# Kernel tuning notes

Hardware: AMD Instinct MI355X
Metric: run time of the kernel (lower is better)

Reference implementation:

```python
import jax, jax.numpy as jnp
import numpy as np

B, N, F_NODE = 4, 50000, 64
E = 1600000
C, F_COL = 1000, 32
H = 16


def setup_inputs() -> dict:
    key = jax.random.key(0)
    ks = jax.random.split(key, 16)
    s = 0.1
    return {
        "node_features": jax.random.normal(ks[0], (B, N, F_NODE), jnp.float32),
        "col_features": jax.random.normal(ks[1], (B, C, F_COL), jnp.float32),
        "edge_index": jax.random.randint(ks[2], (2, E), 0, N, jnp.int32),
        "W1": jax.random.normal(ks[3], (F_NODE, H), jnp.float32) * s,
        "b1": jnp.zeros((H,), jnp.float32),
        "W2": jax.random.normal(ks[4], (H, H), jnp.float32) * s,
        "b2": jnp.zeros((H,), jnp.float32),
        "node_fc_W": jax.random.normal(ks[5], (H, 1), jnp.float32) * s,
        "node_fc_b": jnp.zeros((1,), jnp.float32),
        "col_W1": jax.random.normal(ks[6], (F_COL, H), jnp.float32) * s,
        "col_b1": jnp.zeros((H,), jnp.float32),
        "col_W2": jax.random.normal(ks[7], (H, 1), jnp.float32) * s,
        "col_b2": jnp.zeros((1,), jnp.float32),
        "fc_W": jax.random.normal(ks[8], (2, H), jnp.float32) * s,
        "fc_b": jnp.zeros((H,), jnp.float32),
        "out_W": jax.random.normal(ks[9], (H, 1), jnp.float32) * s,
        "out_b": jnp.zeros((1,), jnp.float32),
    }


def _gcn_conv(x, src, dst, W, b, num_nodes):
    # PyG GCNConv: x' = D^-1/2 (A+I) D^-1/2 (x W) + b
    x = x @ W
    loops = jnp.arange(num_nodes, dtype=src.dtype)
    s = jnp.concatenate([src, loops])
    d = jnp.concatenate([dst, loops])
    deg = jax.ops.segment_sum(jnp.ones_like(d, x.dtype), d, num_segments=num_nodes)
    dinv = jnp.where(deg > 0, jax.lax.rsqrt(deg), 0.0)
    norm = dinv[s] * dinv[d]                     # [E']
    msg = x[s] * norm[:, None]                   # gather + scale
    out = jax.ops.segment_sum(msg, d, num_segments=num_nodes)  # scatter-add
    return out + b


def reference(node_features, col_features, edge_index, W1, b1, W2, b2,
              node_fc_W, node_fc_b, col_W1, col_b1, col_W2, col_b2,
              fc_W, fc_b, out_W, out_b):
    Bs, Nn, Fn = node_features.shape
    num_nodes = Bs * Nn
    x = node_features.reshape(num_nodes, Fn)
    # faithful to torch: edge_index.expand(B,2,E).reshape(2,-1) (indices NOT offset per batch)
    Ee = edge_index.shape[1]
    ei = jnp.broadcast_to(edge_index, (Bs, 2, Ee)).reshape(2, Bs * Ee)
    src, dst = ei[0], ei[1]
    x = jax.nn.relu(_gcn_conv(x, src, dst, W1, b1, num_nodes))
    x = jax.nn.relu(_gcn_conv(x, src, dst, W2, b2, num_nodes))
    x = x.reshape(Bs, Nn, -1)
    node_out = (x @ node_fc_W + node_fc_b)[..., 0]          # [B, N]
    h = jax.nn.relu(col_features @ col_W1 + col_b1)
    col_out = (h @ col_W2 + col_b2)[..., 0]                 # [B, C]
    node_avg = node_out.mean(axis=1)[:, None]               # [B, 1]
    col_avg = col_out.mean(axis=1)[:, None]                 # [B, 1]
    combined = jnp.concatenate([node_avg, col_avg], axis=1)  # [B, 2]
    z = jax.nn.relu(combined @ fc_W + fc_b)
    return z @ out_W + out_b                                # [B, 1]
```

## Files before the change

kernel.cpp:

```cpp
#include <hip/hip_runtime.h>

static constexpr int NN   = 50000;
static constexpr int NBAT = 4;
static constexpr int NE   = 1600000;
static constexpr int NC   = 1000;
static constexpr int FN   = 64;
static constexpr int FCOL = 32;
static constexpr int HD   = 16;

static constexpr int NP     = 20;
static constexpr int PNODES = 2500;
static constexpr int PCAP   = 88000;
static constexpr int NSUB   = 1000;
static constexpr int SNODES = 50;
static constexpr int SCAP   = 2048;
static constexpr int SPP    = 50;
static constexpr int SLICES = 44;
static constexpr int CHUNK  = 4096;
static constexpr int CHUNK2 = 2048;

static constexpr int P1B  = (NE + CHUNK - 1) / CHUNK;
static constexpr int MLPB = (NN + 127) / 128;
static constexpr int COLB = 16;

__device__ inline float block_reduce_256(float v) {
    __shared__ float s[4];
    int lane = threadIdx.x & 63, wid = threadIdx.x >> 6;
    #pragma unroll
    for (int o = 32; o > 0; o >>= 1) v += __shfl_down(v, o);
    if (lane == 0) s[wid] = v;
    __syncthreads();
    if (threadIdx.x == 0) {
        float t = 0.f;
        #pragma unroll
        for (int i = 0; i < 4; i++) t += s[i];
        return t;
    }
    return 0.f;
}

__device__ inline float dot4(float4 a, float4 w) {
    return (a.x * w.x + a.y * w.y) + (a.z * w.z + a.w * w.w);
}

__device__ inline float4 quad_reduce_scatter(const float (&p)[16], int q) {
    constexpr int KA[8] = {0,1,2,3,8,9,10,11};
    constexpr int KB[8] = {4,5,6,7,12,13,14,15};
    bool hi1 = (q & 1);
    float m[8];
    #pragma unroll
    for (int i = 0; i < 8; i++) {
        float send = hi1 ? p[KA[i]] : p[KB[i]];
        float recv = __shfl_xor(send, 1);
        m[i] = (hi1 ? p[KB[i]] : p[KA[i]]) + recv;
    }
    bool hi2 = (q & 2);
    float r0, r1, r2, r3;
    {
        float s0 = hi2 ? m[0] : m[4];
        float s1 = hi2 ? m[1] : m[5];
        float s2 = hi2 ? m[2] : m[6];
        float s3 = hi2 ? m[3] : m[7];
        float v0 = __shfl_xor(s0, 2);
        float v1 = __shfl_xor(s1, 2);
        float v2 = __shfl_xor(s2, 2);
        float v3 = __shfl_xor(s3, 2);
        r0 = (hi2 ? m[4] : m[0]) + v0;
        r1 = (hi2 ? m[5] : m[1]) + v1;
        r2 = (hi2 ? m[6] : m[2]) + v2;
        r3 = (hi2 ? m[7] : m[3]) + v3;
    }
    return make_float4(r0, r1, r2, r3);
}

__device__ inline float mlp_tail(float4 t, int q, bool valid, const float* sw2,
                                 float4 bv, float4 b2v, float4 nfv) {
    float h0 = fmaxf(t.x + bv.x, 0.f);
    float h1 = fmaxf(t.y + bv.y, 0.f);
    float h2 = fmaxf(t.z + bv.z, 0.f);
    float h3 = fmaxf(t.w + bv.w, 0.f);
    float pk[16];
    const float* r0p = &sw2[(q * 4 + 0) * 20];
    const float* r1p = &sw2[(q * 4 + 1) * 20];
    const float* r2p = &sw2[(q * 4 + 2) * 20];
    const float* r3p = &sw2[(q * 4 + 3) * 20];
    #pragma unroll
    for (int k4 = 0; k4 < 4; k4++) {
        float4 w0 = *(const float4*)&r0p[k4 * 4];
        float4 w1 = *(const float4*)&r1p[k4 * 4];
        float4 w2 = *(const float4*)&r2p[k4 * 4];
        float4 w3 = *(const float4*)&r3p[k4 * 4];
        pk[k4*4+0] = h0 * w0.x + h1 * w1.x + h2 * w2.x + h3 * w3.x;
        pk[k4*4+1] = h0 * w0.y + h1 * w1.y + h2 * w2.y + h3 * w3.y;
        pk[k4*4+2] = h0 * w0.z + h1 * w1.z + h2 * w2.z + h3 * w3.z;
        pk[k4*4+3] = h0 * w0.w + h1 * w1.w + h2 * w2.w + h3 * w3.w;
    }
    float4 f = quad_reduce_scatter(pk, q);
    float sv = fmaxf(f.x + b2v.x, 0.f) * nfv.x
             + fmaxf(f.y + b2v.y, 0.f) * nfv.y
             + fmaxf(f.z + b2v.z, 0.f) * nfv.z
             + fmaxf(f.w + b2v.w, 0.f) * nfv.w;
    return valid ? sv : 0.f;
}

__global__ void __launch_bounds__(256) k_mega(
        const float* __restrict__ x, const int* __restrict__ src,
        const int* __restrict__ dst, const float* __restrict__ col,
        const float* __restrict__ W1, const float* __restrict__ b1,
        const float* __restrict__ W2, const float* __restrict__ b2,
        const float* __restrict__ nfcW,
        const float* __restrict__ cW1, const float* __restrict__ cb1,
        const float* __restrict__ cW2,
        int* __restrict__ gcur, unsigned* __restrict__ buf1,
        float* __restrict__ y1, double* __restrict__ sums) {
    __shared__ int ph[NP], pg[NP], pl[NP];
    __shared__ float swt[HD * FN];
    __shared__ float sw2[HD * 20];
    __shared__ float sb1[HD], sb2[HD], snf[HD];
    __shared__ float cw1s[FCOL * HD], csb1[HD], csw2[HD];

    int tid = threadIdx.x;
    int idx = blockIdx.x;

    if (idx < P1B) {
        if (tid < NP) ph[tid] = 0;
        __syncthreads();
        int e0 = idx * CHUNK;
        unsigned ent[16]; int bin[16];
        #pragma unroll
        for (int k = 0; k < 16; k++) {
            int e = e0 + k * 256 + tid;
            if (e < NE) {
                unsigned d = (unsigned)dst[e], s = (unsigned)src[e];
                ent[k] = (d << 16) | s;
                bin[k] = (int)(d / (unsigned)PNODES);
                atomicAdd(&ph[bin[k]], 1);
            } else bin[k] = -1;
        }
        __syncthreads();
        if (tid < NP) { pg[tid] = atomicAdd(&gcur[tid], ph[tid]); pl[tid] = 0; }
        __syncthreads();
        #pragma unroll
        for (int k = 0; k < 16; k++) {
            if (bin[k] >= 0) {
                int p = pg[bin[k]] + atomicAdd(&pl[bin[k]], 1);
                if (p < PCAP) buf1[(size_t)bin[k] * PCAP + p] = ent[k];
            }
        }
        return;
    }

    if (idx < P1B + NBAT * MLPB) {
        int t = idx - P1B;
        int b = t / MLPB, nb = t - b * MLPB;
        int q = tid & 3;
        int n0 = nb * 128 + (tid >> 2) * 2;
        bool v0 = (n0 < NN), v1 = (n0 + 1 < NN);
        const float* xb = x + (size_t)b * NN * FN;

        float4 a0, a1, a2, a3, c0, c1, c2, c3;
        a0 = a1 = a2 = a3 = c0 = c1 = c2 = c3 = make_float4(0.f, 0.f, 0.f, 0.f);
        if (v0) {
            const float4* p = (const float4*)(xb + (size_t)n0 * FN + q * 16);
            a0 = p[0]; a1 = p[1]; a2 = p[2]; a3 = p[3];
        }
        if (v1) {
            const float4* p = (const float4*)(xb + (size_t)(n0 + 1) * FN + q * 16);
            c0 = p[0]; c1 = p[1]; c2 = p[2]; c3 = p[3];
        }

        #pragma unroll
        for (int i = tid; i < HD * FN; i += 256) {
            int j = i >> 6, k = i & 63;
            swt[i] = W1[k * HD + j];
        }
        if (tid < HD * HD) sw2[(tid >> 4) * 20 + (tid & 15)] = W2[tid];
        if (tid < HD) { sb1[tid] = b1[tid]; sb2[tid] = b2[tid]; snf[tid] = nfcW[tid]; }
        __syncthreads();

        float p0[16], p1[16];
        #pragma unroll
        for (int j = 0; j < HD; j++) {
            const float4* w = (const float4*)&swt[j * FN + q * 16];
            float4 w0 = w[0], w1 = w[1], w2 = w[2], w3 = w[3];
            p0[j] = (dot4(a0, w0) + dot4(a1, w1)) + (dot4(a2, w2) + dot4(a3, w3));
            p1[j] = (dot4(c0, w0) + dot4(c1, w1)) + (dot4(c2, w2) + dot4(c3, w3));
        }
        float4 r0 = quad_reduce_scatter(p0, q);
        float4 r1 = quad_reduce_scatter(p1, q);

        if (b == 0) {
            if (v0) *(float4*)&y1[(size_t)n0 * HD + q * 4] = r0;
            if (v1) *(float4*)&y1[(size_t)(n0 + 1) * HD + q * 4] = r1;
        } else {
            float4 bv  = *(const float4*)&sb1[q * 4];
            float4 b2v = *(const float4*)&sb2[q * 4];
            float4 nfv = *(const float4*)&snf[q * 4];
            float sv = mlp_tail(r0, q, v0, sw2, bv, b2v, nfv)
                     + mlp_tail(r1, q, v1, sw2, bv, b2v, nfv);
            float bs = block_reduce_256(sv);
            if (tid == 0) atomicAdd(&sums[b], (double)bs);
        }
        return;
    }

    {
        int t = idx - (P1B + NBAT * MLPB);
        int b = t & 3, chunk = t >> 2;
        for (int i = tid; i < FCOL * HD; i += 256) cw1s[i] = cW1[i];
        if (tid < HD) { csb1[tid] = cb1[tid]; csw2[tid] = cW2[tid]; }
        __syncthreads();
        int c = chunk * 256 + tid;
        float sv = 0.f;
        if (c < NC) {
            const float4* cf = (const float4*)(col + ((size_t)b * NC + c) * FCOL);
            float h[HD];
            #pragma unroll
            for (int j = 0; j < HD; j++) h[j] = csb1[j];
            #pragma unroll
            for (int k4 = 0; k4 < FCOL / 4; k4++) {
                float4 f = cf[k4];
                #pragma unroll
                for (int j = 0; j < HD; j++) {
                    h[j] += f.x * cw1s[(4 * k4 + 0) * HD + j];
                    h[j] += f.y * cw1s[(4 * k4 + 1) * HD + j];
                    h[j] += f.z * cw1s[(4 * k4 + 2) * HD + j];
                    h[j] += f.w * cw1s[(4 * k4 + 3) * HD + j];
                }
            }
            #pragma unroll
            for (int j = 0; j < HD; j++) sv += fmaxf(h[j], 0.f) * csw2[j];
        }
        float bs = block_reduce_256(sv);
        if (tid == 0) atomicAdd(&sums[4 + b], (double)bs);
    }
}

__global__ void __launch_bounds__(256) k_part2(
        const int* __restrict__ gcur, const unsigned* __restrict__ buf1,
        int* __restrict__ cur2, unsigned* __restrict__ buf2) {
    __shared__ int hist[SPP], gbase[SPP], lcur[SPP];
    int part = blockIdx.x / SLICES;
    int slice = blockIdx.x % SLICES;
    int count = min(gcur[part], PCAP);
    int base = slice * CHUNK2;
    if (base >= count) return;
    const unsigned* in = buf1 + (size_t)part * PCAP;
    int sub0 = part * SPP;
    int tid = threadIdx.x;
    if (tid < SPP) hist[tid] = 0;
    __syncthreads();
    unsigned ent[8]; int bin[8];
    #pragma unroll
    for (int k = 0; k < 8; k++) {
        int i = base + k * 256 + tid;
        if (i < count) {
            unsigned e = in[i];
            ent[k] = e;
            bin[k] = (int)((e >> 16) / (unsigned)SNODES) - sub0;
            atomicAdd(&hist[bin[k]], 1);
        } else bin[k] = -1;
    }
    __syncthreads();
    if (tid < SPP) { gbase[tid] = atomicAdd(&cur2[sub0 + tid], hist[tid]); lcur[tid] = 0; }
    __syncthreads();
    #pragma unroll
    for (int k = 0; k < 8; k++) {
        if (bin[k] >= 0) {
            int p = gbase[bin[k]] + atomicAdd(&lcur[bin[k]], 1);
            if (p < SCAP) buf2[(size_t)(sub0 + bin[k]) * SCAP + p] = ent[k];
        }
    }
}

__global__ void __launch_bounds__(256) k_hist(
        const int* __restrict__ cur2, const unsigned* __restrict__ buf2,
        int* __restrict__ cnt, float* __restrict__ dinv, float* __restrict__ z1) {
    __shared__ int hist[SNODES];
    int tid = threadIdx.x, sub = blockIdx.x, vbase = sub * SNODES;
    if (tid < SNODES) hist[tid] = 0;
    __syncthreads();
    int count = min(cur2[sub], SCAP);
    const unsigned* in = buf2 + (size_t)sub * SCAP;
    for (int i = tid; i < count; i += 256)
        atomicAdd(&hist[(int)(in[i] >> 16) - vbase], 1);
    __syncthreads();
    if (tid < SNODES) {
        int c = hist[tid];
        cnt[vbase + tid] = c;
        dinv[vbase + tid] = rsqrtf((float)(4 * c + 1));
    }
    __syncthreads();
    if (tid < SNODES * 4) {
        int vl = tid >> 2, f4 = tid & 3;
        float dv = rsqrtf((float)(4 * hist[vl] + 1));
        float4* p = (float4*)&z1[(size_t)(vbase + vl) * HD + f4 * 4];
        float4 v = *p;
        *p = make_float4(dv * v.x, dv * v.y, dv * v.z, dv * v.w);
    }
}

__device__ inline void sort_sublist(int sub, const int* __restrict__ cur2,
                                    const int* __restrict__ cnt,
                                    const unsigned* __restrict__ buf2,
                                    unsigned* sorted, int* rp, int* cur, int* s) {
    int tid = threadIdx.x, vbase = sub * SNODES;
    int own = (tid < SNODES) ? cnt[vbase + tid] : 0;
    if (tid < 64) s[tid] = own;
    __syncthreads();
    #pragma unroll
    for (int off = 1; off < 64; off <<= 1) {
        int v = (tid < 64 && tid >= off) ? s[tid - off] : 0;
        __syncthreads();
        if (tid < 64) s[tid] += v;
        __syncthreads();
    }
    if (tid < SNODES) {
        int excl = s[tid] - own;
        rp[tid] = excl;
        cur[tid] = excl;
    }
    if (tid == SNODES - 1) rp[SNODES] = s[tid];
    __syncthreads();
    int count = min(cur2[sub], SCAP);
    const unsigned* in = buf2 + (size_t)sub * SCAP;
    for (int i = tid; i < count; i += 256) {
        unsigned e = in[i];
        int p = atomicAdd(&cur[(int)(e >> 16) - vbase], 1);
        sorted[p] = e;
    }
    __syncthreads();
}

__device__ inline void load_sorted(int sub, const int* __restrict__ cur2,
                                   const int* __restrict__ cnt,
                                   const unsigned* __restrict__ buf2,
                                   unsigned* sorted, int* rp, int* s) {
    int tid = threadIdx.x, vbase = sub * SNODES;
    int own = (tid < SNODES) ? cnt[vbase + tid] : 0;
    if (tid < 64) s[tid] = own;
    __syncthreads();
    #pragma unroll
    for (int off = 1; off < 64; off <<= 1) {
        int v = (tid < 64 && tid >= off) ? s[tid - off] : 0;
        __syncthreads();
        if (tid < 64) s[tid] += v;
        __syncthreads();
    }
    if (tid < SNODES) rp[tid] = s[tid] - own;
    if (tid == SNODES - 1) rp[SNODES] = s[tid];
    __syncthreads();
    int count = min(cur2[sub], SCAP);
    const unsigned* in = buf2 + (size_t)sub * SCAP;
    for (int i = tid; i < count; i += 256) sorted[i] = in[i];
    __syncthreads();
}

__device__ inline float gather_run(const unsigned* sorted, int s0, int s1,
                                   const float* __restrict__ z, int j) {
    float acc = 0.f;
    int i = s0;
    for (; i + 4 <= s1; i += 4) {
        unsigned a = sorted[i], b = sorted[i+1], c = sorted[i+2], d = sorted[i+3];
        float va = z[(a & 0xffffu) * HD + j];
        float vb = z[(b & 0xffffu) * HD + j];
        float vc = z[(c & 0xffffu) * HD + j];
        float vd = z[(d & 0xffffu) * HD + j];
        acc += (va + vb) + (vc + vd);
    }
    for (; i < s1; i++) acc += z[(sorted[i] & 0xffffu) * HD + j];
    return acc;
}

__global__ void __launch_bounds__(256) k_conv1(
        const int* __restrict__ cur2, const int* __restrict__ cnt,
        unsigned* __restrict__ buf2,
        const float* __restrict__ dinv, const float* __restrict__ z1,
        const float* __restrict__ b1, const float* __restrict__ W2,
        float* __restrict__ z2) {
    __shared__ unsigned sorted[SCAP];
    __shared__ int rp[SNODES + 1], cur[SNODES], s[64];
    __shared__ float sW[HD * HD], sb[HD];
    int tid = threadIdx.x;
    if (tid < HD * HD) sW[tid] = W2[tid];
    if (tid < HD) sb[tid] = b1[tid];
    int sub = blockIdx.x, vbase = sub * SNODES;
    sort_sublist(sub, cur2, cnt, buf2, sorted, rp, cur, s);

    {
        int count = min(cur2[sub], SCAP);
        unsigned* outp = buf2 + (size_t)sub * SCAP;
        for (int i = tid; i < count; i += 256) outp[i] = sorted[i];
    }

    int j = tid & 15, g = tid >> 4;
    int sbase = (tid & 63) & 48;
    #pragma unroll
    for (int it = 0; it < (SNODES + 15) / 16; it++) {
        int lv = it * 16 + g;
        bool valid = (lv < SNODES);
        float h = 0.f, dv = 0.f;
        if (valid) {
            float acc = gather_run(sorted, rp[lv], rp[lv + 1], z1, j);
            int v = vbase + lv;
            dv = dinv[v];
            h = fmaxf(4.f * dv * acc + dv * z1[v * HD + j] + sb[j], 0.f);
        }
        float o = 0.f;
        #pragma unroll
        for (int k = 0; k < HD; k++) o += __shfl(h, sbase + k) * sW[k * HD + j];
        if (valid) z2[(vbase + lv) * HD + j] = dv * o;
    }
}

__global__ void __launch_bounds__(256) k_conv2(
        const int* __restrict__ cur2, const int* __restrict__ cnt,
        const unsigned* __restrict__ buf2,
        const float* __restrict__ dinv, const float* __restrict__ z2,
        const float* __restrict__ b2, const float* __restrict__ nfcW,
        double* __restrict__ sums) {
    __shared__ unsigned sorted[SCAP];
    __shared__ int rp[SNODES + 1], s[64];
    __shared__ float sb[HD], sw[HD];
    int tid = threadIdx.x;
    if (tid < HD) { sb[tid] = b2[tid]; sw[tid] = nfcW[tid]; }
    int sub = blockIdx.x, vbase = sub * SNODES;
    load_sorted(sub, cur2, cnt, buf2, sorted, rp, s);

    int j = tid & 15, g = tid >> 4;
    float part = 0.f;
    #pragma unroll
    for (int it = 0; it < (SNODES + 15) / 16; it++) {
        int lv = it * 16 + g;
        if (lv < SNODES) {
            float acc = gather_run(sorted, rp[lv], rp[lv + 1], z2, j);
            int v = vbase + lv;
            float dv = dinv[v];
            float h = fmaxf(4.f * dv * acc + dv * z2[v * HD + j] + sb[j], 0.f);
            part += h * sw[j];
        }
    }
    float bs = block_reduce_256(part);
    if (tid == 0) atomicAdd(&sums[0], (double)bs);
}

__global__ void k_final(const double* __restrict__ sums,
                        const float* __restrict__ nfcb, const float* __restrict__ cb2,
                        const float* __restrict__ fcW, const float* __restrict__ fcb,
                        const float* __restrict__ outW, const float* __restrict__ outb,
                        float* __restrict__ out) {
    int b = threadIdx.x;
    if (b < NBAT) {
        float na = (float)(sums[b] * (1.0 / NN)) + nfcb[0];
        float ca = (float)(sums[4 + b] * (1.0 / NC)) + cb2[0];
        float o = outb[0];
        #pragma unroll
        for (int j = 0; j < HD; j++) {
            float z = fmaxf(na * fcW[j] + ca * fcW[HD + j] + fcb[j], 0.f);
            o += z * outW[j];
        }
        out[b] = o;
    }
}

extern "C" void kernel_launch(void* const* d_in, const int* in_sizes, int n_in,
                              void* d_out, int out_size, void* d_ws, size_t ws_size,
                              hipStream_t stream) {
    const float* x    = (const float*)d_in[0];
    const float* col  = (const float*)d_in[1];
    const int*   ei   = (const int*)d_in[2];
    const float* W1   = (const float*)d_in[3];
    const float* b1   = (const float*)d_in[4];
    const float* W2   = (const float*)d_in[5];
    const float* b2   = (const float*)d_in[6];
    const float* nfcW = (const float*)d_in[7];
    const float* nfcb = (const float*)d_in[8];
    const float* cW1  = (const float*)d_in[9];
    const float* cb1  = (const float*)d_in[10];
    const float* cW2  = (const float*)d_in[11];
    const float* cb2  = (const float*)d_in[12];
    const float* fcW  = (const float*)d_in[13];
    const float* fcb  = (const float*)d_in[14];
    const float* outW = (const float*)d_in[15];
    const float* outb = (const float*)d_in[16];
    float* out = (float*)d_out;

    char* ws = (char*)d_ws;
    int*      gcur = (int*)     (ws + 0);
    int*      cur2 = (int*)     (ws + 128);
    int*      cnt  = (int*)     (ws + 4224);
    float*    dinv = (float*)   (ws + 204224);
    unsigned* buf1 = (unsigned*)(ws + 404480);
    float*    z2   = (float*)   (ws + 404480);
    float*    z1   = (float*)   (ws + 7444480);
    unsigned* buf2 = (unsigned*)(ws + 10644480);
    double*   sums = (double*)  (ws + 18836480);

    const int* src = ei;
    const int* dst = ei + NE;

    hipMemsetAsync(gcur, 0, 4128, stream);
    hipMemsetAsync(sums, 0, 8 * sizeof(double), stream);

    int megaBlocks = P1B + NBAT * MLPB + COLB;
    k_mega <<<megaBlocks, 256, 0, stream>>>(x, src, dst, col, W1, b1, W2, b2,
                                            nfcW, cW1, cb1, cW2, gcur, buf1, z1, sums);
    k_part2<<<NP * SLICES, 256, 0, stream>>>(gcur, buf1, cur2, buf2);
    k_hist <<<NSUB, 256, 0, stream>>>(cur2, buf2, cnt, dinv, z1);
    k_conv1<<<NSUB, 256, 0, stream>>>(cur2, cnt, buf2, dinv, z1, b1, W2, z2);
    k_conv2<<<NSUB, 256, 0, stream>>>(cur2, cnt, buf2, dinv, z2, b2, nfcW, sums);
    k_final<<<1, 64, 0, stream>>>(sums, nfcb, cb2, fcW, fcb, outW, outb, out);
}
```

Measured before the change: 113.5 us.

## Spread per-batch node MLP blocks across the later pipeline kernels

The per-batch node MLP work used to run entirely in the first mega kernel, once per batch. Now batch 0 stays in stage 1 and batches 1-3 are placed as extra blocks in the partition, histogram and conv1 kernels. The aim is to balance load and overlap compute-bound MLP blocks with the memory- and atomic-bound partition and sort stages. Shared memory is now a manually carved char buffer so the two kinds of block can share one kernel. This adds extra blocks to each stage and makes the layout of shared memory offsets harder to maintain.

New measurement: 217.7 us. 1.92x slower.

```diff
diff --git a/kernel.cpp b/kernel.cpp
--- a/kernel.cpp
+++ b/kernel.cpp
@@ -22,6 +22,7 @@
 static constexpr int P1B  = (NE + CHUNK - 1) / CHUNK;
 static constexpr int MLPB = (NN + 127) / 128;
 static constexpr int COLB = 16;
+static constexpr int P2B  = NP * SLICES;
 
 __device__ inline float block_reduce_256(float v) {
     __shared__ float s[4];
@@ -55,22 +56,16 @@
         m[i] = (hi1 ? p[KB[i]] : p[KA[i]]) + recv;
     }
     bool hi2 = (q & 2);
-    float r0, r1, r2, r3;
-    {
-        float s0 = hi2 ? m[0] : m[4];
-        float s1 = hi2 ? m[1] : m[5];
-        float s2 = hi2 ? m[2] : m[6];
-        float s3 = hi2 ? m[3] : m[7];
-        float v0 = __shfl_xor(s0, 2);
-        float v1 = __shfl_xor(s1, 2);
-        float v2 = __shfl_xor(s2, 2);
-        float v3 = __shfl_xor(s3, 2);
-        r0 = (hi2 ? m[4] : m[0]) + v0;
-        r1 = (hi2 ? m[5] : m[1]) + v1;
-        r2 = (hi2 ? m[6] : m[2]) + v2;
-        r3 = (hi2 ? m[7] : m[3]) + v3;
-    }
-    return make_float4(r0, r1, r2, r3);
+    float s0 = hi2 ? m[0] : m[4];
+    float s1 = hi2 ? m[1] : m[5];
+    float s2 = hi2 ? m[2] : m[6];
+    float s3 = hi2 ? m[3] : m[7];
+    float v0 = __shfl_xor(s0, 2);
+    float v1 = __shfl_xor(s1, 2);
+    float v2 = __shfl_xor(s2, 2);
+    float v3 = __shfl_xor(s3, 2);
+    return make_float4((hi2 ? m[4] : m[0]) + v0, (hi2 ? m[5] : m[1]) + v1,
+                       (hi2 ? m[6] : m[2]) + v2, (hi2 ? m[7] : m[3]) + v3);
 }
 
 __device__ inline float mlp_tail(float4 t, int q, bool valid, const float* sw2,
@@ -103,7 +98,68 @@
     return valid ? sv : 0.f;
 }
 
-__global__ void __launch_bounds__(256) k_mega(
+__device__ inline void mlp_block(int b, int nb, float* smemf,
+        const float* __restrict__ x, const float* __restrict__ W1,
+        const float* __restrict__ b1, const float* __restrict__ W2,
+        const float* __restrict__ b2, const float* __restrict__ nfcW,
+        float* __restrict__ y1, double* __restrict__ sums) {
+    float* swt = smemf;
+    float* sw2 = smemf + 1024;
+    float* sb1 = smemf + 1344;
+    float* sb2 = smemf + 1360;
+    float* snf = smemf + 1376;
+    int tid = threadIdx.x;
+    int q = tid & 3;
+    int n0 = nb * 128 + (tid >> 2) * 2;
+    bool v0 = (n0 < NN), v1 = (n0 + 1 < NN);
+    const float* xb = x + (size_t)b * NN * FN;
+
+    float4 a0, a1, a2, a3, c0, c1, c2, c3;
+    a0 = a1 = a2 = a3 = c0 = c1 = c2 = c3 = make_float4(0.f, 0.f, 0.f, 0.f);
+    if (v0) {
+        const float4* p = (const float4*)(xb + (size_t)n0 * FN + q * 16);
+        a0 = p[0]; a1 = p[1]; a2 = p[2]; a3 = p[3];
+    }
+    if (v1) {
+        const float4* p = (const float4*)(xb + (size_t)(n0 + 1) * FN + q * 16);
+        c0 = p[0]; c1 = p[1]; c2 = p[2]; c3 = p[3];
+    }
+
+    #pragma unroll
+    for (int i = tid; i < HD * FN; i += 256) {
+        int j = i >> 6, k = i & 63;
+        swt[i] = W1[k * HD + j];
+    }
+    if (tid < HD * HD) sw2[(tid >> 4) * 20 + (tid & 15)] = W2[tid];
+    if (tid < HD) { sb1[tid] = b1[tid]; sb2[tid] = b2[tid]; snf[tid] = nfcW[tid]; }
+    __syncthreads();
+
+    float p0[16], p1[16];
+    #pragma unroll
+    for (int j = 0; j < HD; j++) {
+        const float4* w = (const float4*)&swt[j * FN + q * 16];
+        float4 w0 = w[0], w1 = w[1], w2 = w[2], w3 = w[3];
+        p0[j] = (dot4(a0, w0) + dot4(a1, w1)) + (dot4(a2, w2) + dot4(a3, w3));
+        p1[j] = (dot4(c0, w0) + dot4(c1, w1)) + (dot4(c2, w2) + dot4(c3, w3));
+    }
+    float4 r0 = quad_reduce_scatter(p0, q);
+    float4 r1 = quad_reduce_scatter(p1, q);
+
+    if (b == 0) {
+        if (v0) *(float4*)&y1[(size_t)n0 * HD + q * 4] = r0;
+        if (v1) *(float4*)&y1[(size_t)(n0 + 1) * HD + q * 4] = r1;
+    } else {
+        float4 bv  = *(const float4*)&sb1[q * 4];
+        float4 b2v = *(const float4*)&sb2[q * 4];
+        float4 nfv = *(const float4*)&snf[q * 4];
+        float sv = mlp_tail(r0, q, v0, sw2, bv, b2v, nfv)
+                 + mlp_tail(r1, q, v1, sw2, bv, b2v, nfv);
+        float bs = block_reduce_256(sv);
+        if (tid == 0) atomicAdd(&sums[b], (double)bs);
+    }
+}
+
+__global__ void __launch_bounds__(256) k_stage1(
         const float* __restrict__ x, const int* __restrict__ src,
         const int* __restrict__ dst, const float* __restrict__ col,
         const float* __restrict__ W1, const float* __restrict__ b1,
@@ -113,16 +169,13 @@
         const float* __restrict__ cW2,
         int* __restrict__ gcur, unsigned* __restrict__ buf1,
         float* __restrict__ y1, double* __restrict__ sums) {
-    __shared__ int ph[NP], pg[NP], pl[NP];
-    __shared__ float swt[HD * FN];
-    __shared__ float sw2[HD * 20];
-    __shared__ float sb1[HD], sb2[HD], snf[HD];
-    __shared__ float cw1s[FCOL * HD], csb1[HD], csw2[HD];
-
+    __shared__ __align__(16) char smem[5632];
     int tid = threadIdx.x;
     int idx = blockIdx.x;
 
     if (idx < P1B) {
+        int* pi = (int*)smem;
+        int *ph = pi, *pg = pi + 20, *pl = pi + 40;
         if (tid < NP) ph[tid] = 0;
         __syncthreads();
         int e0 = idx * CHUNK;
@@ -149,63 +202,15 @@
         }
         return;
     }
-
-    if (idx < P1B + NBAT * MLPB) {
-        int t = idx - P1B;
-        int b = t / MLPB, nb = t - b * MLPB;
-        int q = tid & 3;
-        int n0 = nb * 128 + (tid >> 2) * 2;
-        bool v0 = (n0 < NN), v1 = (n0 + 1 < NN);
-        const float* xb = x + (size_t)b * NN * FN;
-
-        float4 a0, a1, a2, a3, c0, c1, c2, c3;
-        a0 = a1 = a2 = a3 = c0 = c1 = c2 = c3 = make_float4(0.f, 0.f, 0.f, 0.f);
-        if (v0) {
-            const float4* p = (const float4*)(xb + (size_t)n0 * FN + q * 16);
-            a0 = p[0]; a1 = p[1]; a2 = p[2]; a3 = p[3];
-        }
-        if (v1) {
-            const float4* p = (const float4*)(xb + (size_t)(n0 + 1) * FN + q * 16);
-            c0 = p[0]; c1 = p[1]; c2 = p[2]; c3 = p[3];
-        }
-
-        #pragma unroll
-        for (int i = tid; i < HD * FN; i += 256) {
-            int j = i >> 6, k = i & 63;
-            swt[i] = W1[k * HD + j];
-        }
-        if (tid < HD * HD) sw2[(tid >> 4) * 20 + (tid & 15)] = W2[tid];
-        if (tid < HD) { sb1[tid] = b1[tid]; sb2[tid] = b2[tid]; snf[tid] = nfcW[tid]; }
-        __syncthreads();
-
-        float p0[16], p1[16];
-        #pragma unroll
-        for (int j = 0; j < HD; j++) {
-            const float4* w = (const float4*)&swt[j * FN + q * 16];
-            float4 w0 = w[0], w1 = w[1], w2 = w[2], w3 = w[3];
-            p0[j] = (dot4(a0, w0) + dot4(a1, w1)) + (dot4(a2, w2) + dot4(a3, w3));
-            p1[j] = (dot4(c0, w0) + dot4(c1, w1)) + (dot4(c2, w2) + dot4(c3, w3));
-        }
-        float4 r0 = quad_reduce_scatter(p0, q);
-        float4 r1 = quad_reduce_scatter(p1, q);
-
-        if (b == 0) {
-            if (v0) *(float4*)&y1[(size_t)n0 * HD + q * 4] = r0;
-            if (v1) *(float4*)&y1[(size_t)(n0 + 1) * HD + q * 4] = r1;
-        } else {
-            float4 bv  = *(const float4*)&sb1[q * 4];
-            float4 b2v = *(const float4*)&sb2[q * 4];
-            float4 nfv = *(const float4*)&snf[q * 4];
-            float sv = mlp_tail(r0, q, v0, sw2, bv, b2v, nfv)
-                     + mlp_tail(r1, q, v1, sw2, bv, b2v, nfv);
-            float bs = block_reduce_256(sv);
-            if (tid == 0) atomicAdd(&sums[b], (double)bs);
-        }
+    if (idx < P1B + MLPB) {
+        mlp_block(0, idx - P1B, (float*)smem, x, W1, b1, W2, b2, nfcW, y1, sums);
         return;
     }
-
     {
-        int t = idx - (P1B + NBAT * MLPB);
+        float* cw1s = (float*)smem;
+        float* csb1 = (float*)smem + 512;
+        float* csw2 = (float*)smem + 528;
+        int t = idx - (P1B + MLPB);
         int b = t & 3, chunk = t >> 2;
         for (int i = tid; i < FCOL * HD; i += 256) cw1s[i] = cW1[i];
         if (tid < HD) { csb1[tid] = cb1[tid]; csw2[tid] = cW2[tid]; }
@@ -236,68 +241,94 @@
     }
 }
 
-__global__ void __launch_bounds__(256) k_part2(
+__global__ void __launch_bounds__(256) k_stage2(
+        const float* __restrict__ x,
+        const float* __restrict__ W1, const float* __restrict__ b1,
+        const float* __restrict__ W2, const float* __restrict__ b2,
+        const float* __restrict__ nfcW,
         const int* __restrict__ gcur, const unsigned* __restrict__ buf1,
-        int* __restrict__ cur2, unsigned* __restrict__ buf2) {
-    __shared__ int hist[SPP], gbase[SPP], lcur[SPP];
-    int part = blockIdx.x / SLICES;
-    int slice = blockIdx.x % SLICES;
-    int count = min(gcur[part], PCAP);
-    int base = slice * CHUNK2;
-    if (base >= count) return;
-    const unsigned* in = buf1 + (size_t)part * PCAP;
-    int sub0 = part * SPP;
+        int* __restrict__ cur2, unsigned* __restrict__ buf2,
+        double* __restrict__ sums) {
+    __shared__ __align__(16) char smem[5632];
     int tid = threadIdx.x;
-    if (tid < SPP) hist[tid] = 0;
-    __syncthreads();
-    unsigned ent[8]; int bin[8];
-    #pragma unroll
-    for (int k = 0; k < 8; k++) {
-        int i = base + k * 256 + tid;
-        if (i < count) {
-            unsigned e = in[i];
-            ent[k] = e;
-            bin[k] = (int)((e >> 16) / (unsigned)SNODES) - sub0;
-            atomicAdd(&hist[bin[k]], 1);
-        } else bin[k] = -1;
-    }
-    __syncthreads();
-    if (tid < SPP) { gbase[tid] = atomicAdd(&cur2[sub0 + tid], hist[tid]); lcur[tid] = 0; }
-    __syncthreads();
-    #pragma unroll
-    for (int k = 0; k < 8; k++) {
-        if (bin[k] >= 0) {
-            int p = gbase[bin[k]] + atomicAdd(&lcur[bin[k]], 1);
-            if (p < SCAP) buf2[(size_t)(sub0 + bin[k]) * SCAP + p] = ent[k];
-        }
-    }
-}
-
-__global__ void __launch_bounds__(256) k_hist(
+    int idx = blockIdx.x;
+
+    if (idx < P2B) {
+        int* pi = (int*)smem;
+        int *hist = pi, *gbase = pi + 50, *lcur = pi + 100;
+        int part = idx / SLICES;
+        int slice = idx % SLICES;
+        int count = min(gcur[part], PCAP);
+        int base = slice * CHUNK2;
+        if (base >= count) return;
+        const unsigned* in = buf1 + (size_t)part * PCAP;
+        int sub0 = part * SPP;
+        if (tid < SPP) hist[tid] = 0;
+        __syncthreads();
+        unsigned ent[8]; int bin[8];
+        #pragma unroll
+        for (int k = 0; k < 8; k++) {
+            int i = base + k * 256 + tid;
+            if (i < count) {
+                unsigned e = in[i];
+                ent[k] = e;
+                bin[k] = (int)((e >> 16) / (unsigned)SNODES) - sub0;
+                atomicAdd(&hist[bin[k]], 1);
+            } else bin[k] = -1;
+        }
+        __syncthreads();
+        if (tid < SPP) { gbase[tid] = atomicAdd(&cur2[sub0 + tid], hist[tid]); lcur[tid] = 0; }
+        __syncthreads();
+        #pragma unroll
+        for (int k = 0; k < 8; k++) {
+            if (bin[k] >= 0) {
+                int p = gbase[bin[k]] + atomicAdd(&lcur[bin[k]], 1);
+                if (p < SCAP) buf2[(size_t)(sub0 + bin[k]) * SCAP + p] = ent[k];
+            }
+        }
+        return;
+    }
+    mlp_block(1, idx - P2B, (float*)smem, x, W1, b1, W2, b2, nfcW, (float*)0, sums);
+}
+
+__global__ void __launch_bounds__(256) k_stage3(
+        const float* __restrict__ x,
+        const float* __restrict__ W1, const float* __restrict__ b1,
+        const float* __restrict__ W2, const float* __restrict__ b2,
+        const float* __restrict__ nfcW,
         const int* __restrict__ cur2, const unsigned* __restrict__ buf2,
-        int* __restrict__ cnt, float* __restrict__ dinv, float* __restrict__ z1) {
-    __shared__ int hist[SNODES];
-    int tid = threadIdx.x, sub = blockIdx.x, vbase = sub * SNODES;
-    if (tid < SNODES) hist[tid] = 0;
-    __syncthreads();
-    int count = min(cur2[sub], SCAP);
-    const unsigned* in = buf2 + (size_t)sub * SCAP;
-    for (int i = tid; i < count; i += 256)
-        atomicAdd(&hist[(int)(in[i] >> 16) - vbase], 1);
-    __syncthreads();
-    if (tid < SNODES) {
-        int c = hist[tid];
-        cnt[vbase + tid] = c;
-        dinv[vbase + tid] = rsqrtf((float)(4 * c + 1));
-    }
-    __syncthreads();
-    if (tid < SNODES * 4) {
-        int vl = tid >> 2, f4 = tid & 3;
-        float dv = rsqrtf((float)(4 * hist[vl] + 1));
-        float4* p = (float4*)&z1[(size_t)(vbase + vl) * HD + f4 * 4];
-        float4 v = *p;
-        *p = make_float4(dv * v.x, dv * v.y, dv * v.z, dv * v.w);
-    }
+        int* __restrict__ cnt, float* __restrict__ dinv, float* __restrict__ z1,
+        double* __restrict__ sums) {
+    __shared__ __align__(16) char smem[5632];
+    int tid = threadIdx.x;
+    int idx = blockIdx.x;
+
+    if (idx < NSUB) {
+        int* hist = (int*)smem;
+        int sub = idx, vbase = sub * SNODES;
+        if (tid < SNODES) hist[tid] = 0;
+        __syncthreads();
+        int count = min(cur2[sub], SCAP);
+        const unsigned* in = buf2 + (size_t)sub * SCAP;
+        for (int i = tid; i < count; i += 256)
+            atomicAdd(&hist[(int)(in[i] >> 16) - vbase], 1);
+        __syncthreads();
+        if (tid < SNODES) {
+            int c = hist[tid];
+            cnt[vbase + tid] = c;
+            dinv[vbase + tid] = rsqrtf((float)(4 * c + 1));
+        }
+        __syncthreads();
+        if (tid < SNODES * 4) {
+            int vl = tid >> 2, f4 = tid & 3;
+            float dv = rsqrtf((float)(4 * hist[vl] + 1));
+            float4* p = (float4*)&z1[(size_t)(vbase + vl) * HD + f4 * 4];
+            float4 v = *p;
+            *p = make_float4(dv * v.x, dv * v.y, dv * v.z, dv * v.w);
+        }
+        return;
+    }
+    mlp_block(2, idx - NSUB, (float*)smem, x, W1, b1, W2, b2, nfcW, (float*)0, sums);
 }
 
 __device__ inline void sort_sublist(int sub, const int* __restrict__ cur2,
@@ -372,45 +403,58 @@
     return acc;
 }
 
-__global__ void __launch_bounds__(256) k_conv1(
+__global__ void __launch_bounds__(256) k_stage4(
+        const float* __restrict__ x,
+        const float* __restrict__ W1, const float* __restrict__ b1,
+        const float* __restrict__ W2, const float* __restrict__ b2,
+        const float* __restrict__ nfcW,
         const int* __restrict__ cur2, const int* __restrict__ cnt,
         unsigned* __restrict__ buf2,
         const float* __restrict__ dinv, const float* __restrict__ z1,
-        const float* __restrict__ b1, const float* __restrict__ W2,
-        float* __restrict__ z2) {
-    __shared__ unsigned sorted[SCAP];
-    __shared__ int rp[SNODES + 1], cur[SNODES], s[64];
-    __shared__ float sW[HD * HD], sb[HD];
+        float* __restrict__ z2, double* __restrict__ sums) {
+    __shared__ __align__(16) char smem[10240];
     int tid = threadIdx.x;
-    if (tid < HD * HD) sW[tid] = W2[tid];
-    if (tid < HD) sb[tid] = b1[tid];
-    int sub = blockIdx.x, vbase = sub * SNODES;
-    sort_sublist(sub, cur2, cnt, buf2, sorted, rp, cur, s);
-
-    {
-        int count = min(cur2[sub], SCAP);
-        unsigned* outp = buf2 + (size_t)sub * SCAP;
-        for (int i = tid; i < count; i += 256) outp[i] = sorted[i];
-    }
-
-    int j = tid & 15, g = tid >> 4;
-    int sbase = (tid & 63) & 48;
-    #pragma unroll
-    for (int it = 0; it < (SNODES + 15) / 16; it++) {
-        int lv = it * 16 + g;
-        bool valid = (lv < SNODES);
-        float h = 0.f, dv = 0.f;
-        if (valid) {
-            float acc = gather_run(sorted, rp[lv], rp[lv + 1], z1, j);
-            int v = vbase + lv;
-            dv = dinv[v];
-            h = fmaxf(4.f * dv * acc + dv * z1[v * HD + j] + sb[j], 0.f);
-        }
-        float o = 0.f;
-        #pragma unroll
-        for (int k = 0; k < HD; k++) o += __shfl(h, sbase + k) * sW[k * HD + j];
-        if (valid) z2[(vbase + lv) * HD + j] = dv * o;
-    }
+    int idx = blockIdx.x;
+
+    if (idx < NSUB) {
+        unsigned* sorted = (unsigned*)smem;
+        int* rp  = (int*)(smem + 8192);
+        int* cur = (int*)(smem + 8396);
+        int* s   = (int*)(smem + 8596);
+        float* sW = (float*)(smem + 8852);
+        float* sb = (float*)(smem + 9876);
+        if (tid < HD * HD) sW[tid] = W2[tid];
+        if (tid < HD) sb[tid] = b1[tid];
+        int sub = idx, vbase = sub * SNODES;
+        sort_sublist(sub, cur2, cnt, buf2, sorted, rp, cur, s);
+
+        {
+            int count = min(cur2[sub], SCAP);
+            unsigned* outp = buf2 + (size_t)sub * SCAP;
+            for (int i = tid; i < count; i += 256) outp[i] = sorted[i];
+        }
+
+        int j = tid & 15, g = tid >> 4;
+        int sbase = (tid & 63) & 48;
+        #pragma unroll
+        for (int it = 0; it < (SNODES + 15) / 16; it++) {
+            int lv = it * 16 + g;
+            bool valid = (lv < SNODES);
+            float h = 0.f, dv = 0.f;
+            if (valid) {
+                float acc = gather_run(sorted, rp[lv], rp[lv + 1], z1, j);
+                int v = vbase + lv;
+                dv = dinv[v];
+                h = fmaxf(4.f * dv * acc + dv * z1[v * HD + j] + sb[j], 0.f);
+            }
+            float o = 0.f;
+            #pragma unroll
+            for (int k = 0; k < HD; k++) o += __shfl(h, sbase + k) * sW[k * HD + j];
+            if (valid) z2[(vbase + lv) * HD + j] = dv * o;
+        }
+        return;
+    }
+    mlp_block(3, idx - NSUB, (float*)smem, x, W1, b1, W2, b2, nfcW, (float*)0, sums);
 }
 
 __global__ void __launch_bounds__(256) k_conv2(
@@ -502,12 +546,14 @@
     hipMemsetAsync(gcur, 0, 4128, stream);
     hipMemsetAsync(sums, 0, 8 * sizeof(double), stream);
 
-    int megaBlocks = P1B + NBAT * MLPB + COLB;
-    k_mega <<<megaBlocks, 256, 0, stream>>>(x, src, dst, col, W1, b1, W2, b2,
-                                            nfcW, cW1, cb1, cW2, gcur, buf1, z1, sums);
-    k_part2<<<NP * SLICES, 256, 0, stream>>>(gcur, buf1, cur2, buf2);
-    k_hist <<<NSUB, 256, 0, stream>>>(cur2, buf2, cnt, dinv, z1);
-    k_conv1<<<NSUB, 256, 0, stream>>>(cur2, cnt, buf2, dinv, z1, b1, W2, z2);
-    k_conv2<<<NSUB, 256, 0, stream>>>(cur2, cnt, buf2, dinv, z2, b2, nfcW, sums);
-    k_final<<<1, 64, 0, stream>>>(sums, nfcb, cb2, fcW, fcb, outW, outb, out);
-}
+    k_stage1<<<P1B + MLPB + COLB, 256, 0, stream>>>(x, src, dst, col, W1, b1, W2, b2,
+                                                    nfcW, cW1, cb1, cW2, gcur, buf1, z1, sums);
+    k_stage2<<<P2B + MLPB, 256, 0, stream>>>(x, W1, b1, W2, b2, nfcW,
+                                             gcur, buf1, cur2, buf2, sums);
+    k_stage3<<<NSUB + MLPB, 256, 0, stream>>>(x, W1, b1, W2, b2, nfcW,
+                                              cur2, buf2, cnt, dinv, z1, sums);
+    k_stage4<<<NSUB + MLPB, 256, 0, stream>>>(x, W1, b1, W2, b2, nfcW,
+                                              cur2, cnt, buf2, dinv, z1, z2, sums);
+    k_conv2 <<<NSUB, 256, 0, stream>>>(cur2, cnt, buf2, dinv, z2, b2, nfcW, sums);
+    k_final <<<1, 64, 0, stream>>>(sums, nfcb, cb2, fcW, fcb, outW, outb, out);
+}
```
